# Optimization experiments

Hardware: AMD Instinct MI355X
Metric: run time of the kernel (lower is better)

Reference implementation:

```python
import jax, jax.numpy as jnp
import numpy as np

NUM_HEADS = 16
ROPE_BASE = 10000.0


def _rope_cos_sin(seq_len, head_dim, dtype):
    inv_freq = 1.0 / (ROPE_BASE ** (jnp.arange(0, head_dim, 2, dtype=jnp.float32) / head_dim))
    freqs = jnp.arange(seq_len, dtype=jnp.float32)[:, None] * inv_freq[None, :]  # [L, hd/2]
    return jnp.cos(freqs).astype(dtype), jnp.sin(freqs).astype(dtype)


def _apply_rope(t, cos, sin):
    # t: [B, H, L, hd]; cos/sin: [L, hd/2] broadcast over B,H
    x1 = t[..., ::2]
    x2 = t[..., 1::2]
    r1 = x1 * cos - x2 * sin
    r2 = x1 * sin + x2 * cos
    return jnp.stack([r1, r2], axis=-1).reshape(t.shape)


def setup_inputs() -> dict:
    key = jax.random.key(0)
    k1, k2, k3 = jax.random.split(key, 3)
    B, L, D = 2, 2048, 1024
    x = jax.random.normal(k1, (B, L, D), dtype=jnp.float32)
    W_qkv = jax.random.normal(k2, (3 * D, D), dtype=jnp.float32) * (D ** -0.5)
    W_out = jax.random.normal(k3, (D, D), dtype=jnp.float32) * (D ** -0.5)
    return {"x": x, "W_qkv": W_qkv, "W_out": W_out}


def reference(x, W_qkv, W_out):
    B, L, D = x.shape
    H = NUM_HEADS
    hd = D // H
    scale = hd ** -0.5

    qkv = x @ W_qkv.T                              # [B, L, 3D]
    qkv = qkv.reshape(B, L, 3, H, hd)
    qkv = jnp.transpose(qkv, (2, 0, 3, 1, 4))      # [3, B, H, L, hd]
    q, k, v = qkv[0], qkv[1], qkv[2]

    cos, sin = _rope_cos_sin(L, hd, x.dtype)
    q = _apply_rope(q, cos, sin)
    k = _apply_rope(k, cos, sin)

    logits = jnp.einsum("bhqd,bhkd->bhqk", q, k) * scale
    attn = jax.nn.softmax(logits, axis=-1)         # dropout p=0.0 -> identity
    out = jnp.einsum("bhqk,bhkd->bhqd", attn, v)   # [B, H, L, hd]
    out = jnp.transpose(out, (0, 2, 1, 3)).reshape(B, L, D)
    return out @ W_out.T
```

## Files before the change

kernel.cpp:

```cpp
#include <hip/hip_runtime.h>
#include <hip/hip_bf16.h>
#include <stdint.h>


typedef __bf16 bf16x8 __attribute__((ext_vector_type(8)));
typedef __bf16 bf16x4v __attribute__((ext_vector_type(4)));
typedef float f32x4 __attribute__((ext_vector_type(4)));

__device__ __forceinline__ unsigned short f2bf(float f) {
  union { float f; unsigned int u; } v; v.f = f;
  unsigned int r = v.u + 0x7FFFu + ((v.u >> 16) & 1u);
  return (unsigned short)(r >> 16);
}
__device__ __forceinline__ float b2f(unsigned short u) {
  union { unsigned int u; float f; } v; v.u = ((unsigned int)u) << 16;
  return v.f;
}

__device__ __forceinline__ void gl2lds16(const void* gptr, void* lptr) {
  __builtin_amdgcn_global_load_lds(
      (const __attribute__((address_space(1))) unsigned int*)gptr,
      (__attribute__((address_space(3))) unsigned int*)lptr, 16, 0, 0);
}

__global__ void cvt_all(const float4* __restrict__ x,
                        const float4* __restrict__ wq,
                        const float4* __restrict__ wo,
                        ushort4* __restrict__ xb,
                        ushort4* __restrict__ wqb,
                        ushort4* __restrict__ wob) {
  int i = blockIdx.x * 256 + threadIdx.x;
  float4 v; ushort4* dst; int j;
  if (i < 1048576)      { v = x[i];            dst = xb;  j = i; }
  else if (i < 1835008) { v = wq[i - 1048576]; dst = wqb; j = i - 1048576; }
  else                  { v = wo[i - 1835008]; dst = wob; j = i - 1835008; }
  ushort4 o;
  o.x = f2bf(v.x); o.y = f2bf(v.y); o.z = f2bf(v.z); o.w = f2bf(v.w);
  dst[j] = o;
}

template<int OUT_BF16>
__global__ __launch_bounds__(256) void gemm_bt(
    const __hip_bfloat16* __restrict__ A,
    const __hip_bfloat16* __restrict__ B,
    void* __restrict__ C, int M, int N, int K) {
  __shared__ __align__(16) __hip_bfloat16 As[128 * 32];
  __shared__ __align__(16) __hip_bfloat16 Bs[128 * 32];
  const int tid = threadIdx.x;
  const int lane = tid & 63;
  const int wave = tid >> 6;
  const int wm = (wave >> 1) * 64, wn = (wave & 1) * 64;
  const int g = lane >> 4, lr = lane & 15;
  const int m0 = blockIdx.y * 128, n0 = blockIdx.x * 128;
  f32x4 acc[4][4] = {};

  const char* Ag = (const char*)(A + (size_t)m0 * K);
  const char* Bg = (const char*)(B + (size_t)n0 * K);
  const size_t ldb = (size_t)K * 2;

  for (int kt = 0; kt < K; kt += 32) {
    const char* Ak = Ag + (size_t)kt * 2;
    const char* Bk = Bg + (size_t)kt * 2;
#pragma unroll
    for (int j = 0; j < 2; ++j) {
      int c = tid + j * 256;
      int row = c >> 2;
      int colb = (c & 3) * 16;
      gl2lds16(Ak + (size_t)row * ldb + colb, (char*)As + c * 16);
      gl2lds16(Bk + (size_t)row * ldb + colb, (char*)Bs + c * 16);
    }
    asm volatile("s_waitcnt vmcnt(0)" ::: "memory");
    __syncthreads();
    bf16x8 af[4], bfr[4];
#pragma unroll
    for (int i = 0; i < 4; ++i)
      af[i] = *(const bf16x8*)((const char*)As + (size_t)(wm + i * 16 + lr) * 64 + g * 16);
#pragma unroll
    for (int i = 0; i < 4; ++i)
      bfr[i] = *(const bf16x8*)((const char*)Bs + (size_t)(wn + i * 16 + lr) * 64 + g * 16);
#pragma unroll
    for (int i = 0; i < 4; ++i)
#pragma unroll
      for (int j = 0; j < 4; ++j)
        acc[i][j] = __builtin_amdgcn_mfma_f32_16x16x32_bf16(af[i], bfr[j], acc[i][j], 0, 0, 0);
    __syncthreads();
  }

#pragma unroll
  for (int i = 0; i < 4; ++i) {
#pragma unroll
    for (int j = 0; j < 4; ++j) {
      int n = n0 + wn + j * 16 + lr;
#pragma unroll
      for (int r = 0; r < 4; ++r) {
        int m = m0 + wm + i * 16 + g * 4 + r;
        float v = acc[i][j][r];
        if (OUT_BF16) {
          ((unsigned short*)C)[(size_t)m * N + n] = f2bf(v);
        } else {
          ((float*)C)[(size_t)m * N + n] = v;
        }
      }
    }
  }
}

__global__ void rope_scatter(const __hip_bfloat16* __restrict__ qkv,
                             __hip_bfloat16* __restrict__ Qs,
                             __hip_bfloat16* __restrict__ Ks,
                             __hip_bfloat16* __restrict__ Vt) {
  const int t = blockIdx.x * 256 + threadIdx.x;
  const int i = t & 31;
  const int lc = (t >> 5) & 255;
  const int h = (t >> 13) & 15;
  const int b = t >> 17;
  const float inv_freq = powf(10000.0f, -(float)i * (1.0f / 32.0f));
  const float QSCALE = 0.125f * 1.44269504088896f;
  const unsigned short* qk = (const unsigned short*)qkv;
  unsigned short v0[8], v1[8];
#pragma unroll
  for (int j = 0; j < 8; ++j) {
    const int l = lc * 8 + j;
    const size_t row = ((size_t)(b * 2048 + l)) * 3072;
    float s, c;
    sincosf((float)l * inv_freq, &s, &c);
    ushort2 qp = *(const ushort2*)(qk + row + h * 64 + 2 * i);
    ushort2 kp = *(const ushort2*)(qk + row + 1024 + h * 64 + 2 * i);
    ushort2 vp = *(const ushort2*)(qk + row + 2048 + h * 64 + 2 * i);
    float x1 = b2f(qp.x), x2 = b2f(qp.y);
    float y1 = b2f(kp.x), y2 = b2f(kp.y);
    size_t oidx = (((size_t)(b * 16 + h)) * 2048 + l) * 64 + 2 * i;
    ushort2 qo, ko;
    qo.x = f2bf((x1 * c - x2 * s) * QSCALE);
    qo.y = f2bf((x1 * s + x2 * c) * QSCALE);
    ko.x = f2bf(y1 * c - y2 * s);
    ko.y = f2bf(y1 * s + y2 * c);
    *(ushort2*)((unsigned short*)Qs + oidx) = qo;
    *(ushort2*)((unsigned short*)Ks + oidx) = ko;
    v0[j] = vp.x; v1[j] = vp.y;
  }
  unsigned short* Vtu = (unsigned short*)Vt;
  const size_t vrow0 = (((size_t)(b * 16 + h)) * 64 + 2 * i) * 2048 + lc * 8;
  const size_t vrow1 = vrow0 + 2048;
  *(ushort4*)(Vtu + vrow0)     = make_ushort4(v0[0], v0[1], v0[2], v0[3]);
  *(ushort4*)(Vtu + vrow0 + 4) = make_ushort4(v0[4], v0[5], v0[6], v0[7]);
  *(ushort4*)(Vtu + vrow1)     = make_ushort4(v1[0], v1[1], v1[2], v1[3]);
  *(ushort4*)(Vtu + vrow1 + 4) = make_ushort4(v1[4], v1[5], v1[6], v1[7]);
}

__global__ __launch_bounds__(256, 7) void attn_fwd(
    const __hip_bfloat16* __restrict__ Qs,
    const __hip_bfloat16* __restrict__ Ks,
    const __hip_bfloat16* __restrict__ Vt,
    float* __restrict__ Opart,
    float2* __restrict__ Ml) {
  constexpr int L = 2048;
  __shared__ __align__(16) __hip_bfloat16 Kt[64 * 64];
  __shared__ __align__(16) __hip_bfloat16 Vts[64 * 64];
  const int tid = threadIdx.x, lane = tid & 63, w = tid >> 6;
  const int g = lane >> 4, lr = lane & 15;
  const int blk = blockIdx.x;
  const int xcd = blk & 7, slot = blk >> 3;
  const int bh = xcd * 4 + (slot >> 6);
  const int r6 = slot & 63;
  const int qt = r6 >> 1, half = r6 & 1;
  const int q = qt * 64 + w * 16 + lr;
  const int kt0 = half * 16;

  const __hip_bfloat16* Qrow = Qs + ((size_t)bh * L + q) * 64;
  bf16x8 qf0 = *(const bf16x8*)(Qrow + g * 8);
  bf16x8 qf1 = *(const bf16x8*)(Qrow + 32 + g * 8);

  const int mask = (lr & 7) << 4;
  const int kb0 = lr * 128 + ((g * 16) ^ (mask & 0x30)) + (mask & 0x40);
  const int kb1 = kb0 ^ 64;
  const int pw0 = w * 2048 + lr * 128 + ((g * 8) ^ (mask & 0x10));
  const int q60 = mask & 0x60;

  const int c0 = tid * 16, c1 = c0 + 4096;
  const int osA = c0 ^ (((c0 >> 7) & 7) << 4);
  const int osB = c1 ^ (((c1 >> 7) & 7) << 4);
  const char* KsrcA = (const char*)(Ks + (size_t)bh * L * 64) + (size_t)kt0 * 8192 + osA;
  const char* KsrcB = (const char*)(Ks + (size_t)bh * L * 64) + (size_t)kt0 * 8192 + osB;
  const char* Vg = (const char*)(Vt + (size_t)bh * 64 * L) + (size_t)kt0 * 128;
  const char* VsrcA = Vg + (size_t)(osA >> 7) * (L * 2) + (osA & 127);
  const char* VsrcB = Vg + (size_t)(osB >> 7) * (L * 2) + (osB & 127);

  f32x4 oacc[4] = {};
  float mrun = -1e30f, lpart = 0.0f;

  for (int kt = 0; kt < 16; ++kt) {
    gl2lds16(KsrcA, (char*)Kt + c0);
    gl2lds16(KsrcB, (char*)Kt + c1);
    gl2lds16(VsrcA, (char*)Vts + c0);
    gl2lds16(VsrcB, (char*)Vts + c1);
    KsrcA += 8192; KsrcB += 8192; VsrcA += 128; VsrcB += 128;
    asm volatile("s_waitcnt vmcnt(0)" ::: "memory");
    asm volatile("s_barrier" ::: "memory");

    f32x4 sacc[4] = {};
#pragma unroll
    for (int mf = 0; mf < 4; ++mf) {
      bf16x8 a0 = *(const bf16x8*)((const char*)Kt + kb0 + mf * 2048);
      bf16x8 a1 = *(const bf16x8*)((const char*)Kt + kb1 + mf * 2048);
      sacc[mf] = __builtin_amdgcn_mfma_f32_16x16x32_bf16(a0, qf0, sacc[mf], 0, 0, 0);
      sacc[mf] = __builtin_amdgcn_mfma_f32_16x16x32_bf16(a1, qf1, sacc[mf], 0, 0, 0);
    }
    asm volatile("s_waitcnt lgkmcnt(0)" ::: "memory");
    asm volatile("s_barrier" ::: "memory");

    float t0 = fmaxf(fmaxf(sacc[0][0], sacc[0][1]), fmaxf(sacc[0][2], sacc[0][3]));
    float t1 = fmaxf(fmaxf(sacc[1][0], sacc[1][1]), fmaxf(sacc[1][2], sacc[1][3]));
    float t2 = fmaxf(fmaxf(sacc[2][0], sacc[2][1]), fmaxf(sacc[2][2], sacc[2][3]));
    float t3 = fmaxf(fmaxf(sacc[3][0], sacc[3][1]), fmaxf(sacc[3][2], sacc[3][3]));
    float tmax = fmaxf(fmaxf(t0, t1), fmaxf(t2, t3));
    tmax = fmaxf(tmax, __shfl_xor(tmax, 16));
    tmax = fmaxf(tmax, __shfl_xor(tmax, 32));
    if (__any(tmax > mrun + 8.0f)) {
      float mnew = fmaxf(mrun, tmax);
      float al = __builtin_amdgcn_exp2f(mrun - mnew);
      mrun = mnew;
      lpart *= al;
#pragma unroll
      for (int d = 0; d < 4; ++d) oacc[d] = oacc[d] * al;
    }
#pragma unroll
    for (int mf = 0; mf < 4; ++mf) {
      float p0 = __builtin_amdgcn_exp2f(sacc[mf][0] - mrun);
      float p1 = __builtin_amdgcn_exp2f(sacc[mf][1] - mrun);
      float p2 = __builtin_amdgcn_exp2f(sacc[mf][2] - mrun);
      float p3 = __builtin_amdgcn_exp2f(sacc[mf][3] - mrun);
      lpart += (p0 + p1) + (p2 + p3);
      bf16x4v pk = { (__bf16)p0, (__bf16)p1, (__bf16)p2, (__bf16)p3 };
      *(bf16x4v*)((char*)Kt + (pw0 + (q60 ^ (mf * 32)))) = pk;
    }

#pragma unroll
    for (int ks = 0; ks < 2; ++ks) {
      const int kb = ks ? kb1 : kb0;
      bf16x8 pf = *(const bf16x8*)((const char*)Kt + w * 2048 + kb);
#pragma unroll
      for (int df = 0; df < 4; ++df) {
        bf16x8 a = *(const bf16x8*)((const char*)Vts + kb + df * 2048);
        oacc[df] = __builtin_amdgcn_mfma_f32_16x16x32_bf16(a, pf, oacc[df], 0, 0, 0);
      }
    }
    asm volatile("s_waitcnt lgkmcnt(0)" ::: "memory");
    asm volatile("s_barrier" ::: "memory");
  }

  lpart += __shfl_xor(lpart, 16);
  lpart += __shfl_xor(lpart, 32);

  const size_t rowi = ((size_t)bh * L + q) * 2 + half;
  float* Od = Opart + rowi * 64;
#pragma unroll
  for (int df = 0; df < 4; ++df)
    *(f32x4*)(Od + df * 16 + g * 4) = oacc[df];
  if (g == 0) {
    float2 ml; ml.x = mrun; ml.y = lpart;
    Ml[rowi] = ml;
  }
}

__global__ __launch_bounds__(256) void attn_reduce(
    const float* __restrict__ Opart, const float2* __restrict__ Ml,
    unsigned short* __restrict__ Ob) {
  int t = blockIdx.x * 256 + threadIdx.x;
  int d = t & 63;
  int r = t >> 6;
  float2 a = Ml[2 * r], b = Ml[2 * r + 1];
  float m = fmaxf(a.x, b.x);
  float w0 = __builtin_amdgcn_exp2f(a.x - m);
  float w1 = __builtin_amdgcn_exp2f(b.x - m);
  float l = a.y * w0 + b.y * w1;
  float o = Opart[(size_t)(2 * r) * 64 + d] * w0 + Opart[(size_t)(2 * r + 1) * 64 + d] * w1;
  float out = o / l;
  int bh = r >> 11, qq = r & 2047;
  Ob[(((size_t)(bh >> 4) * 2048 + qq)) * 1024 + (bh & 15) * 64 + d] = f2bf(out);
}

extern "C" void kernel_launch(void* const* d_in, const int* in_sizes, int n_in,
                              void* d_out, int out_size, void* d_ws, size_t ws_size,
                              hipStream_t stream) {
  (void)in_sizes; (void)n_in; (void)out_size; (void)ws_size;
  const float* x    = (const float*)d_in[0];
  const float* wqkv = (const float*)d_in[1];
  const float* wout = (const float*)d_in[2];

  char* ws = (char*)d_ws;
  auto* wob   = (__hip_bfloat16*)(ws + ((size_t)0u  << 20));
  auto* Qsb   = (__hip_bfloat16*)(ws + ((size_t)2u  << 20));
  auto* Ob    = (__hip_bfloat16*)(ws + ((size_t)2u  << 20));
  auto* Ksb   = (__hip_bfloat16*)(ws + ((size_t)10u << 20));
  auto* Vtb   = (__hip_bfloat16*)(ws + ((size_t)18u << 20));
  auto* qkvb  = (__hip_bfloat16*)(ws + ((size_t)26u << 20));
  auto* Opart = (float*)         (ws + ((size_t)26u << 20));
  auto* xb    = (__hip_bfloat16*)(ws + ((size_t)50u << 20));
  auto* wqb   = (__hip_bfloat16*)(ws + ((size_t)58u << 20));
  auto* Mlp   = (float2*)        (ws + ((size_t)58u << 20));

  cvt_all<<<8192, 256, 0, stream>>>((const float4*)x, (const float4*)wqkv,
                                    (const float4*)wout,
                                    (ushort4*)xb, (ushort4*)wqb, (ushort4*)wob);
  gemm_bt<1><<<dim3(24, 32), 256, 0, stream>>>(xb, wqb, (void*)qkvb, 4096, 3072, 1024);
  rope_scatter<<<1024, 256, 0, stream>>>(qkvb, Qsb, Ksb, Vtb);
  attn_fwd<<<2048, 256, 0, stream>>>(Qsb, Ksb, Vtb, Opart, Mlp);
  attn_reduce<<<16384, 256, 0, stream>>>(Opart, Mlp, (unsigned short*)Ob);
  gemm_bt<0><<<dim3(8, 32), 256, 0, stream>>>(Ob, wob, d_out, 4096, 1024, 1024);
}
```

Before: 161.0 us.

## Double-buffer K/V tiles and process 32 query rows per wave in attention

The attention kernel now uses 512-thread blocks, each covering 256 query rows, and every wave handles two 16-row query groups, so each K/V tile loaded into LDS is reused by twice as many queries. K/V tiles are double-buffered in dynamic LDS, with the next tile's global-to-LDS load issued before computing on the current one. The P matrix gets its own LDS region instead of overwriting the K tile, which removes one barrier per iteration. The cost is 64KB of LDS per block, more registers per wave (two accumulator sets), and a grid of only 512 blocks.

```diff
diff --git a/kernel.cpp b/kernel.cpp
--- a/kernel.cpp
+++ b/kernel.cpp
@@ -148,118 +148,141 @@
   *(ushort4*)(Vtu + vrow1 + 4) = make_ushort4(v1[4], v1[5], v1[6], v1[7]);
 }
 
-__global__ __launch_bounds__(256, 7) void attn_fwd(
+__global__ __launch_bounds__(512, 4) void attn_fwd(
     const __hip_bfloat16* __restrict__ Qs,
     const __hip_bfloat16* __restrict__ Ks,
     const __hip_bfloat16* __restrict__ Vt,
     float* __restrict__ Opart,
     float2* __restrict__ Ml) {
   constexpr int L = 2048;
-  __shared__ __align__(16) __hip_bfloat16 Kt[64 * 64];
-  __shared__ __align__(16) __hip_bfloat16 Vts[64 * 64];
+  extern __shared__ __align__(16) char lds[];
   const int tid = threadIdx.x, lane = tid & 63, w = tid >> 6;
   const int g = lane >> 4, lr = lane & 15;
   const int blk = blockIdx.x;
   const int xcd = blk & 7, slot = blk >> 3;
-  const int bh = xcd * 4 + (slot >> 6);
-  const int r6 = slot & 63;
-  const int qt = r6 >> 1, half = r6 & 1;
-  const int q = qt * 64 + w * 16 + lr;
+  const int bh = xcd * 4 + (slot >> 4);
+  const int rem = slot & 15;
+  const int qt = rem >> 1, half = rem & 1;
+  const int q0 = qt * 256 + w * 32 + lr;
   const int kt0 = half * 16;
 
-  const __hip_bfloat16* Qrow = Qs + ((size_t)bh * L + q) * 64;
-  bf16x8 qf0 = *(const bf16x8*)(Qrow + g * 8);
-  bf16x8 qf1 = *(const bf16x8*)(Qrow + 32 + g * 8);
-
-  const int mask = (lr & 7) << 4;
-  const int kb0 = lr * 128 + ((g * 16) ^ (mask & 0x30)) + (mask & 0x40);
-  const int kb1 = kb0 ^ 64;
-  const int pw0 = w * 2048 + lr * 128 + ((g * 8) ^ (mask & 0x10));
-  const int q60 = mask & 0x60;
-
-  const int c0 = tid * 16, c1 = c0 + 4096;
-  const int osA = c0 ^ (((c0 >> 7) & 7) << 4);
-  const int osB = c1 ^ (((c1 >> 7) & 7) << 4);
-  const char* KsrcA = (const char*)(Ks + (size_t)bh * L * 64) + (size_t)kt0 * 8192 + osA;
-  const char* KsrcB = (const char*)(Ks + (size_t)bh * L * 64) + (size_t)kt0 * 8192 + osB;
-  const char* Vg = (const char*)(Vt + (size_t)bh * 64 * L) + (size_t)kt0 * 128;
-  const char* VsrcA = Vg + (size_t)(osA >> 7) * (L * 2) + (osA & 127);
-  const char* VsrcB = Vg + (size_t)(osB >> 7) * (L * 2) + (osB & 127);
-
-  f32x4 oacc[4] = {};
-  float mrun = -1e30f, lpart = 0.0f;
+  const __hip_bfloat16* Qr = Qs + ((size_t)bh * L + q0) * 64;
+  bf16x8 qf[2][2];
+  qf[0][0] = *(const bf16x8*)(Qr + g * 8);
+  qf[0][1] = *(const bf16x8*)(Qr + 32 + g * 8);
+  qf[1][0] = *(const bf16x8*)(Qr + 16 * 64 + g * 8);
+  qf[1][1] = *(const bf16x8*)(Qr + 16 * 64 + 32 + g * 8);
+
+  const int xmask = (lr & 7) << 4;
+  const int loff0 = ((g * 16) ^ (xmask & 0x30)) + (xmask & 0x40);
+  const int loff1 = loff0 ^ 64;
+  const int kb0 = lr * 128 + loff0;
+  const int kb1 = lr * 128 + loff1;
+  char* Pme = lds + 32768 + w * 4096 + lr * 128;
+  const int pwoff = (g * 8) ^ (xmask & 0x10);
+  const int pm = xmask & 0x60;
+
+  const int c0 = tid * 16;
+  const int os = c0 ^ (((c0 >> 7) & 7) << 4);
+  const char* Ksrc = (const char*)(Ks + (size_t)bh * L * 64) + (size_t)kt0 * 8192 + os;
+  const char* Vsrc = (const char*)(Vt + (size_t)bh * 64 * L) +
+                     (size_t)(os >> 7) * (L * 2) + kt0 * 128 + (os & 127);
+
+  auto stage = [&](int bo) {
+    gl2lds16(Ksrc, lds + bo + c0);
+    gl2lds16(Vsrc, lds + 16384 + bo + c0);
+    Ksrc += 8192; Vsrc += 128;
+  };
+
+  f32x4 oacc[2][4] = {};
+  float mrun[2] = {-1e30f, -1e30f}, lpart[2] = {0.0f, 0.0f};
+
+  stage(0);
 
   for (int kt = 0; kt < 16; ++kt) {
-    gl2lds16(KsrcA, (char*)Kt + c0);
-    gl2lds16(KsrcB, (char*)Kt + c1);
-    gl2lds16(VsrcA, (char*)Vts + c0);
-    gl2lds16(VsrcB, (char*)Vts + c1);
-    KsrcA += 8192; KsrcB += 8192; VsrcA += 128; VsrcB += 128;
-    asm volatile("s_waitcnt vmcnt(0)" ::: "memory");
+    const int bo = (kt & 1) * 8192;
+    if (kt + 1 < 16) {
+      stage(bo ^ 8192);
+      asm volatile("s_waitcnt vmcnt(2)" ::: "memory");
+    } else {
+      asm volatile("s_waitcnt vmcnt(0)" ::: "memory");
+    }
     asm volatile("s_barrier" ::: "memory");
 
-    f32x4 sacc[4] = {};
+    const char* Kc = lds + bo;
+    const char* Vc = lds + 16384 + bo;
+
+    f32x4 sacc[2][4] = {};
 #pragma unroll
     for (int mf = 0; mf < 4; ++mf) {
-      bf16x8 a0 = *(const bf16x8*)((const char*)Kt + kb0 + mf * 2048);
-      bf16x8 a1 = *(const bf16x8*)((const char*)Kt + kb1 + mf * 2048);
-      sacc[mf] = __builtin_amdgcn_mfma_f32_16x16x32_bf16(a0, qf0, sacc[mf], 0, 0, 0);
-      sacc[mf] = __builtin_amdgcn_mfma_f32_16x16x32_bf16(a1, qf1, sacc[mf], 0, 0, 0);
+      bf16x8 a0 = *(const bf16x8*)(Kc + kb0 + mf * 2048);
+      bf16x8 a1 = *(const bf16x8*)(Kc + kb1 + mf * 2048);
+      sacc[0][mf] = __builtin_amdgcn_mfma_f32_16x16x32_bf16(a0, qf[0][0], sacc[0][mf], 0, 0, 0);
+      sacc[0][mf] = __builtin_amdgcn_mfma_f32_16x16x32_bf16(a1, qf[0][1], sacc[0][mf], 0, 0, 0);
+      sacc[1][mf] = __builtin_amdgcn_mfma_f32_16x16x32_bf16(a0, qf[1][0], sacc[1][mf], 0, 0, 0);
+      sacc[1][mf] = __builtin_amdgcn_mfma_f32_16x16x32_bf16(a1, qf[1][1], sacc[1][mf], 0, 0, 0);
+    }
+
+#pragma unroll
+    for (int qg = 0; qg < 2; ++qg) {
+      float t0 = fmaxf(fmaxf(sacc[qg][0][0], sacc[qg][0][1]), fmaxf(sacc[qg][0][2], sacc[qg][0][3]));
+      float t1 = fmaxf(fmaxf(sacc[qg][1][0], sacc[qg][1][1]), fmaxf(sacc[qg][1][2], sacc[qg][1][3]));
+      float t2 = fmaxf(fmaxf(sacc[qg][2][0], sacc[qg][2][1]), fmaxf(sacc[qg][2][2], sacc[qg][2][3]));
+      float t3 = fmaxf(fmaxf(sacc[qg][3][0], sacc[qg][3][1]), fmaxf(sacc[qg][3][2], sacc[qg][3][3]));
+      float tmax = fmaxf(fmaxf(t0, t1), fmaxf(t2, t3));
+      tmax = fmaxf(tmax, __shfl_xor(tmax, 16));
+      tmax = fmaxf(tmax, __shfl_xor(tmax, 32));
+      if (__any(tmax > mrun[qg] + 8.0f)) {
+        float mnew = fmaxf(mrun[qg], tmax);
+        float al = __builtin_amdgcn_exp2f(mrun[qg] - mnew);
+        mrun[qg] = mnew;
+        lpart[qg] *= al;
+#pragma unroll
+        for (int d = 0; d < 4; ++d) oacc[qg][d] = oacc[qg][d] * al;
+      }
+#pragma unroll
+      for (int mf = 0; mf < 4; ++mf) {
+        float p0 = __builtin_amdgcn_exp2f(sacc[qg][mf][0] - mrun[qg]);
+        float p1 = __builtin_amdgcn_exp2f(sacc[qg][mf][1] - mrun[qg]);
+        float p2 = __builtin_amdgcn_exp2f(sacc[qg][mf][2] - mrun[qg]);
+        float p3 = __builtin_amdgcn_exp2f(sacc[qg][mf][3] - mrun[qg]);
+        lpart[qg] += (p0 + p1) + (p2 + p3);
+        bf16x4v pk = { (__bf16)p0, (__bf16)p1, (__bf16)p2, (__bf16)p3 };
+        *(bf16x4v*)(Pme + qg * 2048 + pwoff + ((mf * 32) ^ pm)) = pk;
+      }
+    }
+
+#pragma unroll
+    for (int ks = 0; ks < 2; ++ks) {
+      const int lo = ks ? loff1 : loff0;
+      bf16x8 pf0 = *(const bf16x8*)(Pme + lo);
+      bf16x8 pf1 = *(const bf16x8*)(Pme + 2048 + lo);
+#pragma unroll
+      for (int df = 0; df < 4; ++df) {
+        bf16x8 a = *(const bf16x8*)(Vc + (ks ? kb1 : kb0) + df * 2048);
+        oacc[0][df] = __builtin_amdgcn_mfma_f32_16x16x32_bf16(a, pf0, oacc[0][df], 0, 0, 0);
+        oacc[1][df] = __builtin_amdgcn_mfma_f32_16x16x32_bf16(a, pf1, oacc[1][df], 0, 0, 0);
+      }
     }
     asm volatile("s_waitcnt lgkmcnt(0)" ::: "memory");
+    __builtin_amdgcn_sched_barrier(0);
     asm volatile("s_barrier" ::: "memory");
-
-    float t0 = fmaxf(fmaxf(sacc[0][0], sacc[0][1]), fmaxf(sacc[0][2], sacc[0][3]));
-    float t1 = fmaxf(fmaxf(sacc[1][0], sacc[1][1]), fmaxf(sacc[1][2], sacc[1][3]));
-    float t2 = fmaxf(fmaxf(sacc[2][0], sacc[2][1]), fmaxf(sacc[2][2], sacc[2][3]));
-    float t3 = fmaxf(fmaxf(sacc[3][0], sacc[3][1]), fmaxf(sacc[3][2], sacc[3][3]));
-    float tmax = fmaxf(fmaxf(t0, t1), fmaxf(t2, t3));
-    tmax = fmaxf(tmax, __shfl_xor(tmax, 16));
-    tmax = fmaxf(tmax, __shfl_xor(tmax, 32));
-    if (__any(tmax > mrun + 8.0f)) {
-      float mnew = fmaxf(mrun, tmax);
-      float al = __builtin_amdgcn_exp2f(mrun - mnew);
-      mrun = mnew;
-      lpart *= al;
-#pragma unroll
-      for (int d = 0; d < 4; ++d) oacc[d] = oacc[d] * al;
-    }
-#pragma unroll
-    for (int mf = 0; mf < 4; ++mf) {
-      float p0 = __builtin_amdgcn_exp2f(sacc[mf][0] - mrun);
-      float p1 = __builtin_amdgcn_exp2f(sacc[mf][1] - mrun);
-      float p2 = __builtin_amdgcn_exp2f(sacc[mf][2] - mrun);
-      float p3 = __builtin_amdgcn_exp2f(sacc[mf][3] - mrun);
-      lpart += (p0 + p1) + (p2 + p3);
-      bf16x4v pk = { (__bf16)p0, (__bf16)p1, (__bf16)p2, (__bf16)p3 };
-      *(bf16x4v*)((char*)Kt + (pw0 + (q60 ^ (mf * 32)))) = pk;
-    }
-
-#pragma unroll
-    for (int ks = 0; ks < 2; ++ks) {
-      const int kb = ks ? kb1 : kb0;
-      bf16x8 pf = *(const bf16x8*)((const char*)Kt + w * 2048 + kb);
-#pragma unroll
-      for (int df = 0; df < 4; ++df) {
-        bf16x8 a = *(const bf16x8*)((const char*)Vts + kb + df * 2048);
-        oacc[df] = __builtin_amdgcn_mfma_f32_16x16x32_bf16(a, pf, oacc[df], 0, 0, 0);
-      }
-    }
-    asm volatile("s_waitcnt lgkmcnt(0)" ::: "memory");
-    asm volatile("s_barrier" ::: "memory");
-  }
-
-  lpart += __shfl_xor(lpart, 16);
-  lpart += __shfl_xor(lpart, 32);
-
-  const size_t rowi = ((size_t)bh * L + q) * 2 + half;
-  float* Od = Opart + rowi * 64;
-#pragma unroll
-  for (int df = 0; df < 4; ++df)
-    *(f32x4*)(Od + df * 16 + g * 4) = oacc[df];
-  if (g == 0) {
-    float2 ml; ml.x = mrun; ml.y = lpart;
-    Ml[rowi] = ml;
+  }
+
+#pragma unroll
+  for (int qg = 0; qg < 2; ++qg) {
+    float lsum = lpart[qg];
+    lsum += __shfl_xor(lsum, 16);
+    lsum += __shfl_xor(lsum, 32);
+    const size_t rowi = ((size_t)bh * L + q0 + qg * 16) * 2 + half;
+    float* Od = Opart + rowi * 64;
+#pragma unroll
+    for (int df = 0; df < 4; ++df)
+      *(f32x4*)(Od + df * 16 + g * 4) = oacc[qg][df];
+    if (g == 0) {
+      float2 ml; ml.x = mrun[qg]; ml.y = lsum;
+      Ml[rowi] = ml;
+    }
   }
 }
 
@@ -305,7 +328,7 @@
                                     (ushort4*)xb, (ushort4*)wqb, (ushort4*)wob);
   gemm_bt<1><<<dim3(24, 32), 256, 0, stream>>>(xb, wqb, (void*)qkvb, 4096, 3072, 1024);
   rope_scatter<<<1024, 256, 0, stream>>>(qkvb, Qsb, Ksb, Vtb);
-  attn_fwd<<<2048, 256, 0, stream>>>(Qsb, Ksb, Vtb, Opart, Mlp);
+  attn_fwd<<<512, 512, 65536, stream>>>(Qsb, Ksb, Vtb, Opart, Mlp);
   attn_reduce<<<16384, 256, 0, stream>>>(Opart, Mlp, (unsigned short*)Ob);
   gemm_bt<0><<<dim3(8, 32), 256, 0, stream>>>(Ob, wob, d_out, 4096, 1024, 1024);
 }
```

New measurement: 147.0 us. 8.7% less time.
